# Kernel optimization log

Hardware: AMD Instinct MI355X
Metric: run time of the kernel (lower is better)

Reference implementation:

```python
import jax, jax.numpy as jnp
import numpy as np

B, C_IN, C_OUT, T, N, KS = 16, 64, 64, 48, 1024, 3

def setup_inputs() -> dict:
    key = jax.random.key(0)
    k1, k2, k3, k4 = jax.random.split(key, 4)
    x = jax.random.normal(k1, (B, C_IN, T, N), dtype=jnp.float32)
    Lk = jax.random.normal(k2, (KS, N, N), dtype=jnp.float32) / np.sqrt(N)
    # kaiming-uniform-like init for theta, uniform for b
    fan_in = C_IN * KS
    bound_t = np.sqrt(6.0 / fan_in)
    theta = jax.random.uniform(k3, (C_IN, C_OUT, KS), dtype=jnp.float32,
                               minval=-bound_t, maxval=bound_t)
    bound_b = 1.0 / np.sqrt(fan_in)
    b = jax.random.uniform(k4, (1, C_OUT, 1, 1), dtype=jnp.float32,
                           minval=-bound_b, maxval=bound_b)
    return {"x": x, "Lk": Lk, "theta": theta, "b": b}

def reference(x, Lk, theta, b):
    # x: [B, c_in, T, N], Lk: [ks, N, N], theta: [c_in, c_out, ks], b: [1, c_out, 1, 1]
    x_c = jnp.einsum('knm,bitm->bitkn', Lk, x)          # [B, c_in, T, ks, N]
    x_gc = jnp.einsum('iok,bitkn->botn', theta, x_c) + b  # [B, c_out, T, N]
    # Align: c_in == c_out -> identity
    return jax.nn.relu(x_gc + x)
```

## Files before the change

### kernel.cpp

```cpp
#include <hip/hip_runtime.h>
#include <hip/hip_bf16.h>
#include <stdint.h>


typedef short bs8 __attribute__((ext_vector_type(8)));
typedef float f32x4 __attribute__((ext_vector_type(4)));
typedef float f32x16 __attribute__((ext_vector_type(16)));

#define NB   16
#define NC   64
#define NT   48
#define NN   1024
#define NKS  3
#define KDIM 3072
#define KT   48

__device__ __forceinline__ short f2bs(float f) {
  uint32_t u = __builtin_bit_cast(uint32_t, f);
  u = (u + 0x7FFFu + ((u >> 16) & 1u)) >> 16;
  return (short)u;
}

__device__ __forceinline__ void gload16(const void* g, void* l) {
  __builtin_amdgcn_global_load_lds(
      (const __attribute__((address_space(1))) void*)g,
      (__attribute__((address_space(3))) void*)l, 16, 0, 0);
}

__global__ __launch_bounds__(256) void k_prep_bt(const float* __restrict__ Lk,
                                                 short* __restrict__ BT) {
  int gid = blockIdx.x * 256 + threadIdx.x;
  int e = gid * 4;
  int k = e >> 20;
  int rem = e & 1048575;
  int n = rem >> 10;
  int m = rem & 1023;
  float4 v = *reinterpret_cast<const float4*>(Lk + e);
  union { short s[4]; uint64_t u; } p;
  p.s[0] = f2bs(v.x); p.s[1] = f2bs(v.y); p.s[2] = f2bs(v.z); p.s[3] = f2bs(v.w);
  *reinterpret_cast<uint64_t*>(BT + (size_t)n * KDIM + k * NN + m) = p.u;
}

__global__ __launch_bounds__(256, 2) void k_step1(const float* __restrict__ x,
                                                  const float* __restrict__ theta,
                                                  short* __restrict__ Y, int b0) {
  __shared__ __align__(16) short th[NKS * 64 * 72];
  __shared__ __align__(16) float xs[64 * 128];
  int tid = threadIdx.x;
  int wave = tid >> 6;
  for (int idx = tid; idx < NC * NC * NKS; idx += 256) {
    int i = idx / (NC * NKS);
    int r = idx - i * (NC * NKS);
    int o = r / NKS;
    int k = r - o * NKS;
    th[(k * 64 + o) * 72 + i] = f2bs(theta[idx]);
  }

  int bid = blockIdx.x;
  int mt  = bid & 7;
  int btl = bid >> 3;
  int b_l = btl / NT;
  int t   = btl - b_l * NT;
  int b   = b0 + b_l;
  const float* xb = x + (size_t)b * (NC * NT * NN) + (size_t)t * NN + mt * 128;

#pragma unroll
  for (int c = 0; c < 8; ++c) {
    int idx = c * 256 + tid;
    int row = idx >> 5, ch = idx & 31;
    gload16(xb + (size_t)row * (NT * NN) + ch * 4,
            xs + (c * 256 + wave * 64) * 4);
  }
  __syncthreads();

  int lane = tid & 63;
  int l15 = lane & 15, lg = lane >> 4;
  size_t yrow0 = (size_t)btl * 64;

  for (int nni = 0; nni < 2; ++nni) {
    int mloc = wave * 32 + nni * 16 + l15;
    float xv[16];
#pragma unroll
    for (int j = 0; j < 16; ++j) {
      int i = ((j >> 3) << 5) + lg * 8 + (j & 7);
      xv[j] = xs[i * 128 + mloc];
    }
    f32x4 acc[3][4];
#pragma unroll
    for (int k = 0; k < 3; ++k)
#pragma unroll
      for (int mi = 0; mi < 4; ++mi)
        acc[k][mi] = (f32x4){0.f, 0.f, 0.f, 0.f};

#pragma unroll
    for (int ks = 0; ks < 2; ++ks) {
      bs8 bfrag;
#pragma unroll
      for (int j = 0; j < 8; ++j) bfrag[j] = f2bs(xv[ks * 8 + j]);
#pragma unroll
      for (int mi = 0; mi < 4; ++mi) {
#pragma unroll
        for (int k = 0; k < 3; ++k) {
          const bs8* ap = reinterpret_cast<const bs8*>(
              &th[(k * 64 + mi * 16 + l15) * 72 + ks * 32 + lg * 8]);
          acc[k][mi] = __builtin_amdgcn_mfma_f32_16x16x32_bf16(
              *ap, bfrag, acc[k][mi], 0, 0, 0);
        }
      }
    }
    int mcol = mt * 128 + mloc;
#pragma unroll
    for (int k = 0; k < 3; ++k)
#pragma unroll
      for (int mi = 0; mi < 4; ++mi)
#pragma unroll
        for (int q = 0; q < 4; ++q) {
          int o = mi * 16 + lg * 4 + q;
          Y[(yrow0 + o) * KDIM + k * NN + mcol] = f2bs(acc[k][mi][q]);
        }
  }
}


__device__ __forceinline__ void stage_half(const short* __restrict__ src,
                                           short* lds, int h, int tid) {
  int wave = tid >> 6;
#pragma unroll
  for (int r = 0; r < 2; ++r) {
    int idx = h * 1024 + r * 512 + tid;
    int row = idx >> 3, c8 = idx & 7;
    int c8s = c8 ^ (row & 7) ^ ((row >> 3) & 3);
    gload16(src + (size_t)row * KDIM + c8s * 8,
            lds + (h * 1024 + r * 512 + wave * 64) * 8);
  }
}

#define VMC(N) asm volatile("s_waitcnt vmcnt(" #N ")" ::: "memory")
#define BARR() __builtin_amdgcn_s_barrier();

#define READ_A32(DST, MP, P)                                                \
  _Pragma("unroll") for (int e = 0; e < 2; ++e)                             \
    _Pragma("unroll") for (int ks = 0; ks < 4; ++ks) {                      \
      int row = (4 * (MP) + 2 * e + wr) * 32 + l31;                         \
      int ch = (2 * ks + hi) ^ (row & 7) ^ ((row >> 3) & 3);                \
      DST[e][ks] = *(const bs8*)&AL[(P) * 16384 + row * 64 + ch * 8];       \
    }

#define READ_B32(DST, NI, P)                                                \
  _Pragma("unroll") for (int ks = 0; ks < 4; ++ks) {                        \
    int row = (4 * (NI) + wc) * 32 + l31;                                   \
    int ch = (2 * ks + hi) ^ (row & 7) ^ ((row >> 3) & 3);                  \
    DST[ks] = *(const bs8*)&BL[(P) * 16384 + row * 64 + ch * 8];            \
  }

#define COMPUTE32(MP, BF, NI)                                               \
  __builtin_amdgcn_s_setprio(1);                                            \
  _Pragma("unroll") for (int ks = 0; ks < 4; ++ks)                          \
    _Pragma("unroll") for (int e = 0; e < 2; ++e)                           \
      acc[2 * (MP) + e][(NI)] = __builtin_amdgcn_mfma_f32_32x32x16_bf16(    \
          af[e][ks], BF[ks], acc[2 * (MP) + e][(NI)], 0, 0, 0);             \
  __builtin_amdgcn_s_setprio(0);

#define TILE(t, P, S1, S2, VM)                                              \
  {                                                                         \
    bs8 af[2][4], bf0[4], bf1[4];                                           \
    READ_A32(af, 0, P);                                                     \
    READ_B32(bf0, 0, P);                                                    \
    if (S1) stage_half(Yb + ((t) + 1) * 64, AL + ((P) ^ 1) * 16384, 1, tid);\
    BARR();                                                                 \
    COMPUTE32(0, bf0, 0);                                                   \
    READ_B32(bf1, 1, P);                                                    \
    if (S1) stage_half(BTb + ((t) + 1) * 64, BL + ((P) ^ 1) * 16384, 1, tid);\
    BARR();                                                                 \
    COMPUTE32(0, bf1, 1);                                                   \
    READ_A32(af, 1, P);                                                     \
    if (S2) stage_half(Yb + ((t) + 2) * 64, AL + (P) * 16384, 0, tid);      \
    BARR();                                                                 \
    COMPUTE32(1, bf1, 1);                                                   \
    if (S2) stage_half(BTb + ((t) + 2) * 64, BL + (P) * 16384, 0, tid);     \
    VM;                                                                     \
    BARR();                                                                 \
    COMPUTE32(1, bf0, 0);                                                   \
  }

__global__ __launch_bounds__(512, 2) void k_gemm(const short* __restrict__ Y,
                                                 const short* __restrict__ BT,
                                                 const float* __restrict__ x,
                                                 const float* __restrict__ bias,
                                                 float* __restrict__ out,
                                                 int b0, int nwg) {
  __shared__ __align__(16) short AL[2 * 16384];
  __shared__ __align__(16) short BL[2 * 16384];

  int bid = blockIdx.x;
  int cpx = nwg >> 3;
  int swz = (bid & 7) * cpx + (bid >> 3);
  int colb = swz & 3;
  int rowb = swz >> 2;

  int tid = threadIdx.x;
  int lane = tid & 63, wave = tid >> 6;
  int wr = wave >> 2, wc = wave & 3;
  int l31 = lane & 31, hi = lane >> 5;
  int row0 = rowb * 256, col0 = colb * 256;

  const short* Yb  = Y  + (size_t)row0 * KDIM;
  const short* BTb = BT + (size_t)col0 * KDIM;

  f32x16 acc[4][2];
#pragma unroll
  for (int a = 0; a < 4; ++a)
#pragma unroll
    for (int i = 0; i < 2; ++i)
#pragma unroll
      for (int q = 0; q < 16; ++q) acc[a][i][q] = 0.f;

  stage_half(Yb,        AL,         0, tid);
  stage_half(Yb,        AL,         1, tid);
  stage_half(BTb,       BL,         0, tid);
  stage_half(BTb,       BL,         1, tid);
  stage_half(Yb + 64,   AL + 16384, 0, tid);
  stage_half(BTb + 64,  BL + 16384, 0, tid);
  VMC(4);
  BARR();

  for (int t = 0; t < KT - 2; t += 2) {
    TILE(t,     0, 1, 1, VMC(4));
    TILE(t + 1, 1, 1, 1, VMC(4));
  }
  TILE(KT - 2, 0, 1, 0, VMC(0));
  TILE(KT - 1, 1, 0, 0, (void)0);

#pragma unroll
  for (int a = 0; a < 4; ++a) {
    int mf = 2 * a + wr;
#pragma unroll
    for (int q = 0; q < 16; ++q) {
      int r = row0 + mf * 32 + (q & 3) + 8 * (q >> 2) + 4 * hi;
      int o = r & 63;
      int btl = r >> 6;
      int tt = btl % NT;
      int bb = b0 + btl / NT;
      float bo = bias[o];
      size_t obase = ((size_t)(bb * 64 + o) * NT + tt) * NN;
#pragma unroll
      for (int i = 0; i < 2; ++i) {
        int n = col0 + (4 * i + wc) * 32 + l31;
        size_t oidx = obase + n;
        float v = acc[a][i][q] + bo + x[oidx];
        out[oidx] = v > 0.f ? v : 0.f;
      }
    }
  }
}

extern "C" void kernel_launch(void* const* d_in, const int* in_sizes, int n_in,
                              void* d_out, int out_size, void* d_ws, size_t ws_size,
                              hipStream_t stream) {
  const float* x     = (const float*)d_in[0];
  const float* Lk    = (const float*)d_in[1];
  const float* theta = (const float*)d_in[2];
  const float* bias  = (const float*)d_in[3];
  float* out = (float*)d_out;

  char* ws = (char*)d_ws;
  short* BT = (short*)ws;
  short* Y  = (short*)(ws + (size_t)(8u << 20));
  size_t avail = ws_size > ((size_t)8u << 20) ? ws_size - ((size_t)8u << 20) : 0;
  size_t perB = (size_t)NT * NC * KDIM * 2;
  int bc = 16;
  while (bc > 1 && (size_t)bc * perB > avail) bc >>= 1;

  k_prep_bt<<<dim3(3072), dim3(256), 0, stream>>>(Lk, BT);
  for (int b0 = 0; b0 < NB; b0 += bc) {
    k_step1<<<dim3(bc * 384), dim3(256), 0, stream>>>(x, theta, Y, b0);
    int nwg = bc * 48;
    k_gemm<<<dim3(nwg), dim3(512), 0, stream>>>(Y, BT, x, bias, out, b0, nwg);
  }
}
```

Before: 483.5 us.

## Triple-buffer A tiles and collapse GEMM pipeline to one barrier per K-tile

The LDS staging scheme moves from half-tile double buffering with four barriers per K-tile to whole-tile staging. A is triple-buffered and prefetched two tiles ahead, and B is double-buffered and prefetched one tile ahead. Only one barrier is needed per K-step, which cuts synchronisation stalls between MFMA phases and gives loads more time to land. The cost is 32KB more LDS (160KB total), which leaves no headroom for a second workgroup per CU, and longer buffer-reuse distances that rely on careful vmcnt accounting.

```diff
diff --git a/kernel.cpp b/kernel.cpp
--- a/kernel.cpp
+++ b/kernel.cpp
@@ -122,16 +122,14 @@
 }
 
 
-__device__ __forceinline__ void stage_half(const short* __restrict__ src,
-                                           short* lds, int h, int tid) {
-  int wave = tid >> 6;
-#pragma unroll
-  for (int r = 0; r < 2; ++r) {
-    int idx = h * 1024 + r * 512 + tid;
+__device__ __forceinline__ void stage_tile(const short* __restrict__ src,
+                                           short* lds, int tid) {
+#pragma unroll
+  for (int c = 0; c < 4; ++c) {
+    int idx = c * 512 + tid;
     int row = idx >> 3, c8 = idx & 7;
     int c8s = c8 ^ (row & 7) ^ ((row >> 3) & 3);
-    gload16(src + (size_t)row * KDIM + c8s * 8,
-            lds + (h * 1024 + r * 512 + wave * 64) * 8);
+    gload16(src + (size_t)row * KDIM + c8s * 8, lds + idx * 8);
   }
 }
 
@@ -161,26 +159,22 @@
           af[e][ks], BF[ks], acc[2 * (MP) + e][(NI)], 0, 0, 0);             \
   __builtin_amdgcn_s_setprio(0);
 
-#define TILE(t, P, S1, S2, VM)                                              \
+#define TILE(t, PA, PB, SB, SA, VM, BR)                                     \
   {                                                                         \
     bs8 af[2][4], bf0[4], bf1[4];                                           \
-    READ_A32(af, 0, P);                                                     \
-    READ_B32(bf0, 0, P);                                                    \
-    if (S1) stage_half(Yb + ((t) + 1) * 64, AL + ((P) ^ 1) * 16384, 1, tid);\
-    BARR();                                                                 \
+    READ_A32(af, 0, PA);                                                    \
+    READ_B32(bf0, 0, PB);                                                   \
+    if (SB) stage_tile(BTb + ((t) + 1) * 64, BL + ((PB) ^ 1) * 16384, tid); \
+    if (SA) stage_tile(Yb + ((t) + 2) * 64,                                 \
+                       AL + (((PA) + 2) % 3) * 16384, tid);                 \
     COMPUTE32(0, bf0, 0);                                                   \
-    READ_B32(bf1, 1, P);                                                    \
-    if (S1) stage_half(BTb + ((t) + 1) * 64, BL + ((P) ^ 1) * 16384, 1, tid);\
-    BARR();                                                                 \
+    READ_B32(bf1, 1, PB);                                                   \
     COMPUTE32(0, bf1, 1);                                                   \
-    READ_A32(af, 1, P);                                                     \
-    if (S2) stage_half(Yb + ((t) + 2) * 64, AL + (P) * 16384, 0, tid);      \
-    BARR();                                                                 \
+    READ_A32(af, 1, PA);                                                    \
     COMPUTE32(1, bf1, 1);                                                   \
-    if (S2) stage_half(BTb + ((t) + 2) * 64, BL + (P) * 16384, 0, tid);     \
+    COMPUTE32(1, bf0, 0);                                                   \
     VM;                                                                     \
-    BARR();                                                                 \
-    COMPUTE32(1, bf0, 0);                                                   \
+    BR;                                                                     \
   }
 
 __global__ __launch_bounds__(512, 2) void k_gemm(const short* __restrict__ Y,
@@ -189,7 +183,7 @@
                                                  const float* __restrict__ bias,
                                                  float* __restrict__ out,
                                                  int b0, int nwg) {
-  __shared__ __align__(16) short AL[2 * 16384];
+  __shared__ __align__(16) short AL[3 * 16384];
   __shared__ __align__(16) short BL[2 * 16384];
 
   int bid = blockIdx.x;
@@ -215,21 +209,26 @@
 #pragma unroll
       for (int q = 0; q < 16; ++q) acc[a][i][q] = 0.f;
 
-  stage_half(Yb,        AL,         0, tid);
-  stage_half(Yb,        AL,         1, tid);
-  stage_half(BTb,       BL,         0, tid);
-  stage_half(BTb,       BL,         1, tid);
-  stage_half(Yb + 64,   AL + 16384, 0, tid);
-  stage_half(BTb + 64,  BL + 16384, 0, tid);
+  stage_tile(Yb,        AL,         tid);
+  stage_tile(BTb,       BL,         tid);
+  stage_tile(Yb + 64,   AL + 16384, tid);
   VMC(4);
   BARR();
 
-  for (int t = 0; t < KT - 2; t += 2) {
-    TILE(t,     0, 1, 1, VMC(4));
-    TILE(t + 1, 1, 1, 1, VMC(4));
-  }
-  TILE(KT - 2, 0, 1, 0, VMC(0));
-  TILE(KT - 1, 1, 0, 0, (void)0);
+  for (int t = 0; t < 42; t += 6) {
+    TILE(t,     0, 0, 1, 1, VMC(4), BARR());
+    TILE(t + 1, 1, 1, 1, 1, VMC(4), BARR());
+    TILE(t + 2, 2, 0, 1, 1, VMC(4), BARR());
+    TILE(t + 3, 0, 1, 1, 1, VMC(4), BARR());
+    TILE(t + 4, 1, 0, 1, 1, VMC(4), BARR());
+    TILE(t + 5, 2, 1, 1, 1, VMC(4), BARR());
+  }
+  TILE(42, 0, 0, 1, 1, VMC(4), BARR());
+  TILE(43, 1, 1, 1, 1, VMC(4), BARR());
+  TILE(44, 2, 0, 1, 1, VMC(4), BARR());
+  TILE(45, 0, 1, 1, 1, VMC(4), BARR());
+  TILE(46, 1, 0, 1, 0, VMC(0), BARR());
+  TILE(47, 2, 1, 0, 0, (void)0, (void)0);
 
 #pragma unroll
   for (int a = 0; a < 4; ++a) {
```

Measured after the change: 547.3 us. +13.2%, slower.
